# Performance work log

Hardware: AMD Instinct MI355X
Metric: run time of the kernel (lower is better)

Reference implementation:

```python
import jax, jax.numpy as jnp
import numpy as np

N = 100000      # num nodes
E = 3200000     # num edges (avg degree 32)
D = 64          # feature dim
K = 3           # propagation steps (self._k)
ALPHA = 0.1     # convex combine (self._alpha)
EPS = 1e-6      # PNY norm epsilon


def setup_inputs() -> dict:
    key = jax.random.key(0)
    k1, k2, k3 = jax.random.split(key, 3)
    feat = jax.random.normal(k1, (N, D), dtype=jnp.float32)
    src = jax.random.randint(k2, (E,), 0, N)
    dst = jax.random.randint(k3, (E,), 0, N)
    return {"feat": feat, "src": src, "dst": dst}


def reference(feat, src, dst):
    n = feat.shape[0]
    e = src.shape[0]
    ones = jnp.ones((e,), dtype=feat.dtype)
    out_deg = jax.ops.segment_sum(ones, src, num_segments=n)  # [N]
    in_deg = jax.ops.segment_sum(ones, dst, num_segments=n)   # [N]
    src_norm = jnp.power(jnp.clip(out_deg, 1.0, None), -0.5)[:, None]  # [N,1]
    dst_norm = jnp.power(jnp.clip(in_deg, 1.0, None), -0.5)[:, None]   # [N,1]

    feat_0 = feat
    for _ in range(K):
        feat = feat * src_norm                 # degree-norm scale on source side
        prev_x = feat                          # prev_x = clone(feat)
        # u_mul_e('h','w','m') with w==1 + fn.sum: edge-weighted sparse aggregation
        agg = jax.ops.segment_sum(feat[src], dst, num_segments=n)  # [N,D]
        # PNY_Norm(prev_x, agg): per-node L2-norm-preserving rescale of aggregate
        pn = jnp.linalg.norm(prev_x, axis=-1, keepdims=True)
        an = jnp.linalg.norm(agg, axis=-1, keepdims=True)
        feat = agg * (pn / (an + EPS))
        feat = feat * dst_norm                 # degree-norm scale on dest side
        feat = (1.0 - ALPHA) * feat + ALPHA * feat_0  # convex combine with feat_0
    return feat
```

## Files before the change

kernel.cpp:

```cpp
#include <hip/hip_runtime.h>
#include <hip/hip_fp16.h>
#include <math.h>

#define ALPHA 0.1f
#define EPS 1e-6f
#define D 64
#define CH 8192
#define BUCK_SH 8

__global__ void hist_kernel(const int* __restrict__ src, const int* __restrict__ dst,
                            int* __restrict__ hist_d, int* __restrict__ hist_s,
                            int nbuck, int nblk, int E) {
    __shared__ int hd[4][512], hs[4][512];
    int t = threadIdx.x, b = blockIdx.x, w = t >> 6;
    for (int u = t; u < 512; u += 256) {
        hd[0][u] = 0; hd[1][u] = 0; hd[2][u] = 0; hd[3][u] = 0;
        hs[0][u] = 0; hs[1][u] = 0; hs[2][u] = 0; hs[3][u] = 0;
    }
    __syncthreads();
    int beg = b * CH, end = min(beg + CH, E);
    for (int e = beg + t; e < end; e += 256) {
        atomicAdd(&hd[w][dst[e] >> BUCK_SH], 1);
        atomicAdd(&hs[w][src[e] >> BUCK_SH], 1);
    }
    __syncthreads();
    for (int u = t; u < nbuck; u += 256) {
        hist_d[u * nblk + b] = hd[0][u] + hd[1][u] + hd[2][u] + hd[3][u];
        hist_s[u * nblk + b] = hs[0][u] + hs[1][u] + hs[2][u] + hs[3][u];
    }
}

__global__ void bucket_total_kernel(const int* __restrict__ hist_d, const int* __restrict__ hist_s,
                                    int* __restrict__ tot_d, int* __restrict__ tot_s, int nblk) {
    __shared__ int rd[256], rs[256];
    int u = blockIdx.x, t = threadIdx.x;
    int sd = 0, ss = 0;
    for (int b = t; b < nblk; b += 256) {
        sd += hist_d[u * nblk + b];
        ss += hist_s[u * nblk + b];
    }
    rd[t] = sd; rs[t] = ss;
    __syncthreads();
    for (int off = 128; off; off >>= 1) {
        if (t < off) { rd[t] += rd[t + off]; rs[t] += rs[t + off]; }
        __syncthreads();
    }
    if (t == 0) { tot_d[u] = rd[0]; tot_s[u] = rs[0]; }
}

__global__ void base_scan_kernel(const int* __restrict__ tot_d, const int* __restrict__ tot_s,
                                 int* __restrict__ base_d, int* __restrict__ base_s, int nbuck) {
    __shared__ int a[512], b[512];
    int t = threadIdx.x;
    int vd = (t < nbuck) ? tot_d[t] : 0;
    int vs = (t < nbuck) ? tot_s[t] : 0;
    a[t] = vd; b[t] = vs;
    __syncthreads();
    for (int off = 1; off < 512; off <<= 1) {
        int av = (t >= off) ? a[t - off] : 0;
        int bv = (t >= off) ? b[t - off] : 0;
        __syncthreads();
        a[t] += av; b[t] += bv;
        __syncthreads();
    }
    if (t < nbuck) {
        base_d[t] = a[t] - vd;
        base_s[t] = b[t] - vs;
    }
}

__global__ void row_scan_kernel(const int* __restrict__ hist_d, const int* __restrict__ hist_s,
                                const int* __restrict__ base_d, const int* __restrict__ base_s,
                                int* __restrict__ sbase_d, int* __restrict__ sbase_s,
                                int nblk, int E, int m) {
    __shared__ int a[512], b[512];
    int u = blockIdx.x, t = threadIdx.x;
    int hd = (t < nblk) ? hist_d[u * nblk + t] : 0;
    int hs = (t < nblk) ? hist_s[u * nblk + t] : 0;
    a[t] = hd; b[t] = hs;
    __syncthreads();
    for (int off = 1; off < 512; off <<= 1) {
        int av = (t >= off) ? a[t - off] : 0;
        int bv = (t >= off) ? b[t - off] : 0;
        __syncthreads();
        a[t] += av; b[t] += bv;
        __syncthreads();
    }
    if (t < nblk) {
        sbase_d[u * nblk + t] = base_d[u] + a[t] - hd;
        sbase_s[u * nblk + t] = base_s[u] + b[t] - hs;
    }
    if (u == 0 && t == 0) { sbase_d[m] = E; sbase_s[m] = E; }
}

__global__ void scatter_kernel(const int* __restrict__ src, const int* __restrict__ dst,
                               const int* __restrict__ sbase_d, const int* __restrict__ sbase_s,
                               unsigned* __restrict__ pairs, unsigned char* __restrict__ skeys,
                               int nbuck, int nblk, int E) {
    __shared__ unsigned sp[CH];
    __shared__ unsigned char sk[CH];
    __shared__ int hd[512], hs[512];
    __shared__ int ld[512], ls[512];
    __shared__ int ts[256];
    int t = threadIdx.x, b = blockIdx.x;
    for (int u = t; u < 512; u += 256) { hd[u] = 0; hs[u] = 0; }
    __syncthreads();
    int beg = b * CH, end = min(beg + CH, E), cnt = end - beg;
    for (int e = beg + t; e < end; e += 256) {
        atomicAdd(&hd[dst[e] >> BUCK_SH], 1);
        atomicAdd(&hs[src[e] >> BUCK_SH], 1);
    }
    __syncthreads();
    int v0 = hd[2 * t], v1 = hd[2 * t + 1];
    int w0 = hs[2 * t], w1 = hs[2 * t + 1];
    ts[t] = v0 + v1;
    __syncthreads();
    for (int off = 1; off < 256; off <<= 1) {
        int v = (t >= off) ? ts[t - off] : 0;
        __syncthreads();
        ts[t] += v;
        __syncthreads();
    }
    int based = (t == 0) ? 0 : ts[t - 1];
    ld[2 * t] = based; ld[2 * t + 1] = based + v0;
    __syncthreads();
    ts[t] = w0 + w1;
    __syncthreads();
    for (int off = 1; off < 256; off <<= 1) {
        int v = (t >= off) ? ts[t - off] : 0;
        __syncthreads();
        ts[t] += v;
        __syncthreads();
    }
    int bases = (t == 0) ? 0 : ts[t - 1];
    ls[2 * t] = bases; ls[2 * t + 1] = bases + w0;
    __syncthreads();
    hd[2 * t] = ld[2 * t]; hd[2 * t + 1] = ld[2 * t + 1];
    hs[2 * t] = ls[2 * t]; hs[2 * t + 1] = ls[2 * t + 1];
    __syncthreads();
    for (int e = beg + t; e < end; e += 256) {
        int dv = dst[e], sv = src[e];
        int p = atomicAdd(&hd[dv >> BUCK_SH], 1);
        sp[p] = ((unsigned)(dv & 255) << 24) | (unsigned)sv;
        int q = atomicAdd(&hs[sv >> BUCK_SH], 1);
        sk[q] = (unsigned char)(sv & 255);
    }
    __syncthreads();
    for (int i = t; i < cnt; i += 256) {
        unsigned pv = sp[i];
        int lo = 0;
        #pragma unroll
        for (int s = 256; s; s >>= 1) { int mid = lo + s; if (mid < 512 && ld[mid] <= i) lo = mid; }
        pairs[sbase_d[lo * nblk + b] + (i - ld[lo])] = pv;
        unsigned char kv = sk[i];
        int lo2 = 0;
        #pragma unroll
        for (int s = 256; s; s >>= 1) { int mid = lo2 + s; if (mid < 512 && ls[mid] <= i) lo2 = mid; }
        skeys[sbase_s[lo2 * nblk + b] + (i - ls[lo2])] = kv;
    }
}

__global__ void build_kernel(const unsigned* __restrict__ pairs, const int* __restrict__ sbase_d,
                             const unsigned char* __restrict__ skeys, const int* __restrict__ sbase_s,
                             int* __restrict__ rowptr, int* __restrict__ csr,
                             float* __restrict__ dn, float* __restrict__ sn,
                             int nbuck, int nblk, int n, int E) {
    __shared__ int lh[256], le[256], cnt[256], lhs[256];
    int t = threadIdx.x, u = blockIdx.x;
    lh[t] = 0; cnt[t] = 0; lhs[t] = 0;
    __syncthreads();
    int sb = sbase_s[u * nblk];
    int se = sbase_s[(u + 1) * nblk];
    for (int i = sb + t; i < se; i += 256) atomicAdd(&lhs[skeys[i]], 1);
    int beg = sbase_d[u * nblk];
    int end = sbase_d[(u + 1) * nblk];
    for (int i = beg + t; i < end; i += 256) atomicAdd(&lh[pairs[i] >> 24], 1);
    __syncthreads();
    int c0 = lh[t];
    for (int off = 1; off < 256; off <<= 1) {
        int x = (t >= off) ? lh[t - off] : 0;
        __syncthreads();
        lh[t] += x;
        __syncthreads();
    }
    le[t] = lh[t] - c0;
    __syncthreads();
    int node = (u << BUCK_SH) + t;
    if (node < n) {
        rowptr[node] = beg + le[t];
        dn[node] = rsqrtf(fmaxf((float)c0, 1.0f));
        sn[node] = rsqrtf(fmaxf((float)lhs[t], 1.0f));
    }
    if (u == nbuck - 1 && t == 0) rowptr[n] = E;
    for (int i = beg + t; i < end; i += 256) {
        unsigned pr = pairs[i];
        int bb = pr >> 24;
        int p = atomicAdd(&cnt[bb], 1);
        csr[beg + le[bb] + p] = (int)(pr & 0xFFFFFFu);
    }
}

__global__ void prescale_kernel(const float* __restrict__ feat, const float* __restrict__ sn,
                                __half* __restrict__ outh, float* __restrict__ pn, int n) {
    int row  = blockIdx.x * (blockDim.x >> 6) + (threadIdx.x >> 6);
    int lane = threadIdx.x & 63;
    if (row >= n) return;
    float x = feat[(long)row * D + lane];
    float ss = x * x;
    #pragma unroll
    for (int off = 32; off; off >>= 1) ss += __shfl_xor(ss, off, 64);
    float s = sn[row];
    float v = x * s;
    float vp = __shfl_xor(v, 1, 64);
    if (!(lane & 1)) {
        *(__half2*)(outh + (long)row * D + lane) = __floats2half2_rn(v, vp);
    }
    if (lane == 0) pn[row] = s * sqrtf(ss);
}

template <int LAST>
__global__ void iter_kernel(const __half* __restrict__ cur, const float* __restrict__ feat0,
                            const int* __restrict__ rowptr, const int* __restrict__ csr_src,
                            const float* __restrict__ pn, const float* __restrict__ dn,
                            const float* __restrict__ sn,
                            __half* __restrict__ nexth, float* __restrict__ npn,
                            float* __restrict__ out, int n) {
    int row  = blockIdx.x * (blockDim.x >> 6) + (threadIdx.x >> 6);
    int lane = threadIdx.x & 63;
    if (row >= n) return;
    int g = lane >> 3, sub = lane & 7;

    __half2 hz = __float2half2_rn(0.f);
    __half2 hacc0 = hz, hacc1 = hz, hacc2 = hz, hacc3 = hz;
    int beg = rowptr[row], end = rowptr[row + 1];
    for (int base = beg; base < end; base += 64) {
        int m = end - base; if (m > 64) m = 64;
        int s_l = (lane < m) ? csr_src[base + lane] : 0;
        int nfull = m >> 3;
        #pragma unroll 4
        for (int j = 0; j < nfull; ++j) {
            int s = __shfl(s_l, j * 8 + g, 64);
            int4 raw = *(const int4*)(cur + (long)s * D + sub * 8);
            hacc0 = __hadd2(hacc0, *(__half2*)&raw.x);
            hacc1 = __hadd2(hacc1, *(__half2*)&raw.y);
            hacc2 = __hadd2(hacc2, *(__half2*)&raw.z);
            hacc3 = __hadd2(hacc3, *(__half2*)&raw.w);
        }
        int e = nfull * 8 + g;
        int s = __shfl(s_l, e, 64);
        if (e < m) {
            int4 raw = *(const int4*)(cur + (long)s * D + sub * 8);
            hacc0 = __hadd2(hacc0, *(__half2*)&raw.x);
            hacc1 = __hadd2(hacc1, *(__half2*)&raw.y);
            hacc2 = __hadd2(hacc2, *(__half2*)&raw.z);
            hacc3 = __hadd2(hacc3, *(__half2*)&raw.w);
        }
    }
    float acc[8];
    { float2 f; f = __half22float2(hacc0); acc[0] = f.x; acc[1] = f.y;
      f = __half22float2(hacc1); acc[2] = f.x; acc[3] = f.y;
      f = __half22float2(hacc2); acc[4] = f.x; acc[5] = f.y;
      f = __half22float2(hacc3); acc[6] = f.x; acc[7] = f.y; }
    #pragma unroll
    for (int i = 0; i < 8; ++i) {
        float a = acc[i];
        a += __shfl_xor(a, 8, 64);
        a += __shfl_xor(a, 16, 64);
        a += __shfl_xor(a, 32, 64);
        acc[i] = a;
    }
    float dd = 0.f;
    #pragma unroll
    for (int i = 0; i < 8; ++i) dd += acc[i] * acc[i];
    dd += __shfl_xor(dd, 1, 64);
    dd += __shfl_xor(dd, 2, 64);
    dd += __shfl_xor(dd, 4, 64);
    float an = sqrtf(dd);
    float scale = pn[row] / (an + EPS) * dn[row] * (1.0f - ALPHA);

    if (g == 0) {
        long fb = (long)row * D + sub * 8;
        float4 f0a = *(const float4*)(feat0 + fb);
        float4 f0b = *(const float4*)(feat0 + fb + 4);
        float nx[8];
        nx[0] = acc[0] * scale + ALPHA * f0a.x;
        nx[1] = acc[1] * scale + ALPHA * f0a.y;
        nx[2] = acc[2] * scale + ALPHA * f0a.z;
        nx[3] = acc[3] * scale + ALPHA * f0a.w;
        nx[4] = acc[4] * scale + ALPHA * f0b.x;
        nx[5] = acc[5] * scale + ALPHA * f0b.y;
        nx[6] = acc[6] * scale + ALPHA * f0b.z;
        nx[7] = acc[7] * scale + ALPHA * f0b.w;
        if (LAST) {
            float4 o0 = {nx[0], nx[1], nx[2], nx[3]};
            float4 o1 = {nx[4], nx[5], nx[6], nx[7]};
            *(float4*)(out + fb) = o0;
            *(float4*)(out + fb + 4) = o1;
        } else {
            float s = sn[row];
            __half2 h0 = __floats2half2_rn(nx[0] * s, nx[1] * s);
            __half2 h1 = __floats2half2_rn(nx[2] * s, nx[3] * s);
            __half2 h2 = __floats2half2_rn(nx[4] * s, nx[5] * s);
            __half2 h3 = __floats2half2_rn(nx[6] * s, nx[7] * s);
            int4 packed;
            packed.x = *(int*)&h0; packed.y = *(int*)&h1;
            packed.z = *(int*)&h2; packed.w = *(int*)&h3;
            *(int4*)(nexth + fb) = packed;
            float nn = 0.f;
            #pragma unroll
            for (int i = 0; i < 8; ++i) nn += nx[i] * nx[i];
            nn += __shfl_xor(nn, 1, 64);
            nn += __shfl_xor(nn, 2, 64);
            nn += __shfl_xor(nn, 4, 64);
            if (sub == 0) npn[row] = s * sqrtf(nn);
        }
    }
}

extern "C" void kernel_launch(void* const* d_in, const int* in_sizes, int n_in,
                              void* d_out, int out_size, void* d_ws, size_t ws_size,
                              hipStream_t stream) {
    const float* feat = (const float*)d_in[0];
    const int*   src  = (const int*)d_in[1];
    const int*   dst  = (const int*)d_in[2];
    float* out = (float*)d_out;

    int n = in_sizes[0] / D;
    int E = in_sizes[1];

    int nbuck = (n + 255) >> BUCK_SH;
    int nblk  = (E + CH - 1) / CH;
    int m     = nbuck * nblk;

    int* hist_d  = (int*)d_ws;
    int* hist_s  = hist_d + m;
    int* sbase_d = hist_s + m;
    int* sbase_s = sbase_d + m + 1;
    int* tot_d   = sbase_s + m + 1;
    int* tot_s   = tot_d + 512;
    int* base_d  = tot_s + 512;
    int* base_s  = base_d + 512;
    int* rowptr  = base_s + 512;
    float* sn    = (float*)(rowptr + n + 1);
    float* dn    = sn + n;
    float* pn_a  = dn + n;
    float* pn_b  = pn_a + n;

    size_t used4 = (size_t)(4 * m + 2) + 2048 + 5 * (size_t)n + 1;
    size_t offP  = (used4 * 4 + 255) & ~(size_t)255;
    unsigned* pairs  = (unsigned*)((char*)d_ws + offP);
    __half* scaled_a = (__half*)((char*)d_ws + offP);
    __half* scaled_b = scaled_a + (size_t)n * D;
    size_t szP = 2 * (size_t)n * D * sizeof(__half);
    size_t offQ = (offP + szP + 255) & ~(size_t)255;
    unsigned char* skeys = (unsigned char*)d_ws + offQ;
    int* csr = (int*)((char*)d_ws + offQ);

    int eblocks = nblk;
    hist_kernel<<<eblocks, 256, 0, stream>>>(src, dst, hist_d, hist_s, nbuck, nblk, E);
    bucket_total_kernel<<<nbuck, 256, 0, stream>>>(hist_d, hist_s, tot_d, tot_s, nblk);
    base_scan_kernel<<<1, 512, 0, stream>>>(tot_d, tot_s, base_d, base_s, nbuck);
    row_scan_kernel<<<nbuck, 512, 0, stream>>>(hist_d, hist_s, base_d, base_s,
                                               sbase_d, sbase_s, nblk, E, m);
    scatter_kernel<<<eblocks, 256, 0, stream>>>(src, dst, sbase_d, sbase_s, pairs, skeys,
                                                nbuck, nblk, E);
    build_kernel<<<nbuck, 256, 0, stream>>>(pairs, sbase_d, skeys, sbase_s,
                                            rowptr, csr, dn, sn, nbuck, nblk, n, E);

    int blocks = (n + 3) / 4;
    prescale_kernel<<<blocks, 256, 0, stream>>>(feat, sn, scaled_a, pn_a, n);
    iter_kernel<0><<<blocks, 256, 0, stream>>>(scaled_a, feat, rowptr, csr, pn_a, dn, sn,
                                               scaled_b, pn_b, nullptr, n);
    iter_kernel<0><<<blocks, 256, 0, stream>>>(scaled_b, feat, rowptr, csr, pn_b, dn, sn,
                                               scaled_a, pn_a, nullptr, n);
    iter_kernel<1><<<blocks, 256, 0, stream>>>(scaled_a, feat, rowptr, csr, pn_a, dn, sn,
                                               nullptr, nullptr, out, n);
}
```

Before: 301.6 us.

## Process two rows per wavefront in the SpMM iteration kernel

Measured after the change: 295.0 us, median of 2. -2.2%, faster.

```diff
diff --git a/kernel.cpp b/kernel.cpp
--- a/kernel.cpp
+++ b/kernel.cpp
@@ -225,35 +225,36 @@
                             const float* __restrict__ sn,
                             __half* __restrict__ nexth, float* __restrict__ npn,
                             float* __restrict__ out, int n) {
-    int row  = blockIdx.x * (blockDim.x >> 6) + (threadIdx.x >> 6);
+    int wid  = blockIdx.x * (blockDim.x >> 6) + (threadIdx.x >> 6);
     int lane = threadIdx.x & 63;
-    if (row >= n) return;
-    int g = lane >> 3, sub = lane & 7;
+    int half = lane >> 5;
+    int h    = lane & 31;
+    int g    = h >> 3;
+    int sub  = h & 7;
+    int row  = wid * 2 + half;
+    bool valid = row < n;
+
+    int beg = valid ? rowptr[row] : 0;
+    int end = valid ? rowptr[row + 1] : 0;
+    int deg = end - beg;
+    const int* idx = csr_src + beg;
+    unsigned subOff = (unsigned)sub * 16u;
 
     __half2 hz = __float2half2_rn(0.f);
     __half2 hacc0 = hz, hacc1 = hz, hacc2 = hz, hacc3 = hz;
-    int beg = rowptr[row], end = rowptr[row + 1];
-    for (int base = beg; base < end; base += 64) {
-        int m = end - base; if (m > 64) m = 64;
-        int s_l = (lane < m) ? csr_src[base + lane] : 0;
-        int nfull = m >> 3;
-        #pragma unroll 4
-        for (int j = 0; j < nfull; ++j) {
-            int s = __shfl(s_l, j * 8 + g, 64);
-            int4 raw = *(const int4*)(cur + (long)s * D + sub * 8);
-            hacc0 = __hadd2(hacc0, *(__half2*)&raw.x);
-            hacc1 = __hadd2(hacc1, *(__half2*)&raw.y);
-            hacc2 = __hadd2(hacc2, *(__half2*)&raw.z);
-            hacc3 = __hadd2(hacc3, *(__half2*)&raw.w);
-        }
-        int e = nfull * 8 + g;
-        int s = __shfl(s_l, e, 64);
-        if (e < m) {
-            int4 raw = *(const int4*)(cur + (long)s * D + sub * 8);
-            hacc0 = __hadd2(hacc0, *(__half2*)&raw.x);
-            hacc1 = __hadd2(hacc1, *(__half2*)&raw.y);
-            hacc2 = __hadd2(hacc2, *(__half2*)&raw.z);
-            hacc3 = __hadd2(hacc3, *(__half2*)&raw.w);
+    for (int base = 0; base < deg; base += 32) {
+        int s_l = (base + h < deg) ? idx[base + h] : 0;
+        #pragma unroll
+        for (int k = 0; k < 8; ++k) {
+            int e = base + k * 4 + g;
+            int s = __shfl(s_l, (half << 5) | (k * 4 + g), 64);
+            if (e < deg) {
+                int4 raw = *(const int4*)((const char*)cur + (unsigned)s * 128u + subOff);
+                hacc0 = __hadd2(hacc0, *(const __half2*)&raw.x);
+                hacc1 = __hadd2(hacc1, *(const __half2*)&raw.y);
+                hacc2 = __hadd2(hacc2, *(const __half2*)&raw.z);
+                hacc3 = __hadd2(hacc3, *(const __half2*)&raw.w);
+            }
         }
     }
     float acc[8];
@@ -266,7 +267,6 @@
         float a = acc[i];
         a += __shfl_xor(a, 8, 64);
         a += __shfl_xor(a, 16, 64);
-        a += __shfl_xor(a, 32, 64);
         acc[i] = a;
     }
     float dd = 0.f;
@@ -275,6 +275,7 @@
     dd += __shfl_xor(dd, 1, 64);
     dd += __shfl_xor(dd, 2, 64);
     dd += __shfl_xor(dd, 4, 64);
+    if (!valid) return;
     float an = sqrtf(dd);
     float scale = pn[row] / (an + EPS) * dn[row] * (1.0f - ALPHA);
 
@@ -367,12 +368,13 @@
     build_kernel<<<nbuck, 256, 0, stream>>>(pairs, sbase_d, skeys, sbase_s,
                                             rowptr, csr, dn, sn, nbuck, nblk, n, E);
 
-    int blocks = (n + 3) / 4;
-    prescale_kernel<<<blocks, 256, 0, stream>>>(feat, sn, scaled_a, pn_a, n);
-    iter_kernel<0><<<blocks, 256, 0, stream>>>(scaled_a, feat, rowptr, csr, pn_a, dn, sn,
-                                               scaled_b, pn_b, nullptr, n);
-    iter_kernel<0><<<blocks, 256, 0, stream>>>(scaled_b, feat, rowptr, csr, pn_b, dn, sn,
-                                               scaled_a, pn_a, nullptr, n);
-    iter_kernel<1><<<blocks, 256, 0, stream>>>(scaled_a, feat, rowptr, csr, pn_a, dn, sn,
-                                               nullptr, nullptr, out, n);
-}
+    int pblocks = (n + 3) / 4;
+    prescale_kernel<<<pblocks, 256, 0, stream>>>(feat, sn, scaled_a, pn_a, n);
+    int iblocks = ((n + 1) / 2 + 3) / 4;
+    iter_kernel<0><<<iblocks, 256, 0, stream>>>(scaled_a, feat, rowptr, csr, pn_a, dn, sn,
+                                                scaled_b, pn_b, nullptr, n);
+    iter_kernel<0><<<iblocks, 256, 0, stream>>>(scaled_b, feat, rowptr, csr, pn_b, dn, sn,
+                                                scaled_a, pn_a, nullptr, n);
+    iter_kernel<1><<<iblocks, 256, 0, stream>>>(scaled_a, feat, rowptr, csr, pn_a, dn, sn,
+                                                nullptr, nullptr, out, n);
+}
```
